# Kernel optimization log

Measured on AMD Instinct MI355X. Metric: run time of the kernel, lower is better.

The kernel has to match this reference:

```python
import jax, jax.numpy as jnp
import numpy as np

B, N, D, H = 2, 2048, 1024, 16
DH = D // H
SCALE = 1.0 / np.sqrt(DH).astype(np.float32)


def setup_inputs() -> dict:
    key = jax.random.key(0)
    k1, k2, k3, k4, k5 = jax.random.split(key, 5)
    x = jax.random.normal(k1, (B, N, D), dtype=jnp.float32)
    attn_bias = jax.random.normal(k2, (B, N, N), dtype=jnp.float32)
    # valid lengths in [N//2, N]; True = keep
    lengths = jax.random.randint(k3, (B,), N // 2, N + 1)
    key_padding_mask = jnp.arange(N)[None, :] < lengths[:, None]
    Wqkv = jax.random.normal(k4, (3 * D, D), dtype=jnp.float32) / np.sqrt(D)
    Wproj = jax.random.normal(k5, (D, D), dtype=jnp.float32) / np.sqrt(D)
    bproj = jnp.zeros((D,), dtype=jnp.float32)
    return {"x": x, "attn_bias": attn_bias, "key_padding_mask": key_padding_mask,
            "Wqkv": Wqkv, "Wproj": Wproj, "bproj": bproj}


def reference(x, attn_bias, key_padding_mask, Wqkv, Wproj, bproj):
    b, n, d = x.shape
    qkv = x @ Wqkv.T                                   # [B,N,3D]
    qkv = qkv.reshape(b, n, 3, H, DH)
    q = jnp.transpose(qkv[:, :, 0], (0, 2, 1, 3))      # [B,H,N,DH]
    k = jnp.transpose(qkv[:, :, 1], (0, 2, 1, 3))
    v = jnp.transpose(qkv[:, :, 2], (0, 2, 1, 3))
    attn = jnp.einsum('bhnd,bhmd->bhnm', q, k) * SCALE  # [B,H,N,N]
    attn = attn + attn_bias[:, None, :, :]
    attn = jnp.where(key_padding_mask[:, None, None, :], attn, -jnp.inf)
    attn = jax.nn.softmax(attn, axis=-1)
    y = jnp.einsum('bhnm,bhmd->bhnd', attn, v)          # [B,H,N,DH]
    y = jnp.transpose(y, (0, 2, 1, 3)).reshape(b, n, d)
    return y @ Wproj.T + bproj
```

## Files before the change

kernel.cpp:

```cpp
#include <hip/hip_runtime.h>
#include <hip/hip_bf16.h>

namespace {

typedef short short8 __attribute__((ext_vector_type(8)));
typedef float f32x4 __attribute__((ext_vector_type(4)));

__device__ __forceinline__ unsigned short f2bf(float f) {
  union { __hip_bfloat16 h; unsigned short u; } cv;
  cv.h = __float2bfloat16(f);
  return cv.u;
}

__device__ __forceinline__ unsigned cvt_pk_bf16(float lo, float hi) {
  unsigned r;
  asm("v_cvt_pk_bf16_f32 %0, %1, %2" : "=v"(r) : "v"(lo), "v"(hi));
  return r;
}

__device__ __forceinline__ void load_lds16(const void* g, void* l) {
  __builtin_amdgcn_global_load_lds((__attribute__((address_space(1))) void*)g,
                                   (__attribute__((address_space(3))) void*)l,
                                   16, 0, 0);
}

__device__ __forceinline__ int pi64(int rho) {
  const int c32 = rho & 32;
  const int o = (rho >> 4) & 1;
  const int g = (rho >> 2) & 3;
  const int s = rho & 3;
  return c32 + (o ? (((g ^ 2) << 3) + 4 + s) : ((g << 3) + s));
}

__global__ __launch_bounds__(256) void cvt_all(const float4* __restrict__ x,
                                               const float4* __restrict__ wqkv,
                                               const float4* __restrict__ wproj,
                                               ushort4* __restrict__ xb,
                                               ushort4* __restrict__ wqkvb,
                                               ushort4* __restrict__ wprojb) {
  int i = blockIdx.x * 256 + threadIdx.x;
  const float4* src;
  ushort4* dst;
  int off;
  if (i < 1048576) { src = x; dst = xb; off = i; }
  else if (i < 1048576 + 786432) { src = wqkv; dst = wqkvb; off = i - 1048576; }
  else { src = wproj; dst = wprojb; off = i - (1048576 + 786432); }
  float4 f = src[off];
  ushort4 u;
  u.x = f2bf(f.x); u.y = f2bf(f.y); u.z = f2bf(f.z); u.w = f2bf(f.w);
  dst[off] = u;
}

__global__ __launch_bounds__(256) void gemm_qkv(const unsigned short* __restrict__ Xb,
                                                const unsigned short* __restrict__ Wb,
                                                unsigned short* __restrict__ qws,
                                                unsigned short* __restrict__ kws,
                                                unsigned short* __restrict__ vTws) {
  __shared__ unsigned short lA[128 * 32];
  __shared__ unsigned short lB[128 * 32];
  const int t = threadIdx.x;
  const int w = t >> 6, l = t & 63;
  const int wm = w >> 1, wn = w & 1;
  const int lr = l & 15, lg = l >> 4;
  const int row0 = blockIdx.x * 128, col0 = blockIdx.y * 128;
  const int srow = t >> 2;
  const int schunk = (t & 3) ^ (srow & 3);
  f32x4 acc[4][4] = {};
  for (int k0 = 0; k0 < 1024; k0 += 32) {
    __syncthreads();
    load_lds16(Xb + (size_t)(row0 + srow) * 1024 + k0 + schunk * 8, &lA[w * 512]);
    load_lds16(Xb + (size_t)(row0 + 64 + srow) * 1024 + k0 + schunk * 8, &lA[2048 + w * 512]);
    load_lds16(Wb + (size_t)(col0 + srow) * 1024 + k0 + schunk * 8, &lB[w * 512]);
    load_lds16(Wb + (size_t)(col0 + 64 + srow) * 1024 + k0 + schunk * 8, &lB[2048 + w * 512]);
    __syncthreads();
    short8 af[4], bf[4];
    const int rslot = (lg ^ (l & 3)) * 8;
#pragma unroll
    for (int mi = 0; mi < 4; ++mi)
      af[mi] = *(const short8*)&lA[(wm * 64 + mi * 16 + lr) * 32 + rslot];
#pragma unroll
    for (int ni = 0; ni < 4; ++ni)
      bf[ni] = *(const short8*)&lB[(wn * 64 + ni * 16 + lr) * 32 + rslot];
#pragma unroll
    for (int mi = 0; mi < 4; ++mi)
#pragma unroll
      for (int ni = 0; ni < 4; ++ni)
        acc[mi][ni] = __builtin_amdgcn_mfma_f32_16x16x32_bf16(af[mi], bf[ni], acc[mi][ni], 0, 0, 0);
  }
#pragma unroll
  for (int mi = 0; mi < 4; ++mi)
#pragma unroll
    for (int ni = 0; ni < 4; ++ni) {
      const int col = col0 + wn * 64 + ni * 16 + lr;
      const int s = col >> 10, rem = col & 1023;
      const int hh = rem >> 6, dh = rem & 63;
      const int row = row0 + wm * 64 + mi * 16 + lg * 4;
      const int bb = row >> 11, n = row & 2047;
      const size_t bh = (size_t)(bb * 16 + hh);
      if (s == 2) {
        ushort4 u4;
        u4.x = f2bf(acc[mi][ni][0]); u4.y = f2bf(acc[mi][ni][1]);
        u4.z = f2bf(acc[mi][ni][2]); u4.w = f2bf(acc[mi][ni][3]);
        *(ushort4*)&vTws[(bh * 64 + dh) * 2048 + n] = u4;
      } else if (s == 0) {
#pragma unroll
        for (int r = 0; r < 4; ++r)
          qws[(bh * 2048 + n + r) * 64 + dh] = f2bf(acc[mi][ni][r] * 0.125f);
      } else {
#pragma unroll
        for (int r = 0; r < 4; ++r)
          kws[(bh * 2048 + n + r) * 64 + dh] = f2bf(acc[mi][ni][r]);
      }
    }
}

__global__ __launch_bounds__(256, 4) void attn_fwd(const unsigned short* __restrict__ qws,
                                                   const unsigned short* __restrict__ kws,
                                                   const unsigned short* __restrict__ vTws,
                                                   const float* __restrict__ bias,
                                                   const int* __restrict__ mask,
                                                   unsigned short* __restrict__ ctx) {
  __shared__ unsigned short lK[2][64 * 64];
  __shared__ unsigned short lVT[2][64 * 64];
  __shared__ int lred[4];
  const int t = threadIdx.x, w = t >> 6, l = t & 63;
  const int lr = l & 15, lg = l >> 4;
  const int xr7 = lr & 7;

  const int lin = blockIdx.x;
  const int g8 = lin & 7;
  const int k7 = lin >> 3;
  const int h = k7 & 15;
  const int gg = g8 + (k7 >> 4) * 8;
  const int qt = gg >> 1;
  const int b = gg & 1;

  const size_t bh = (size_t)(b * 16 + h);
  const unsigned short* Q = qws + bh * (2048 * 64);
  const unsigned short* K = kws + bh * (2048 * 64);
  const unsigned short* VT = vTws + bh * (64 * 2048);
  const float* brow = bias + (size_t)b * (2048 * 2048);

  const int* mrow = mask + b * 2048;
  int scnt = 0;
  for (int i = t; i < 2048; i += 256) scnt += (mrow[i] != 0);
#pragma unroll
  for (int d = 1; d < 64; d <<= 1) scnt += __shfl_xor(scnt, d, 64);
  if (l == 0) lred[w] = scnt;
  __syncthreads();
  const int len = lred[0] + lred[1] + lred[2] + lred[3];
  const int nt = (len + 63) >> 6;

  const int qv = qt * 64 + w * 16 + lr;
  short8 qf[2];
  qf[0] = *(const short8*)&Q[(size_t)qv * 64 + lg * 8];
  qf[1] = *(const short8*)&Q[(size_t)qv * 64 + 32 + lg * 8];
  const float* bq = brow + (size_t)qv * 2048;

  const int be = lg * 8, bo = ((lg ^ 2) * 8) + 4;
  const int boffs[4] = {be, bo, 32 + be, 32 + bo};

  float m = -INFINITY, lsum = 0.f;
  f32x4 o[4] = {};

  const int sr = l >> 3;
  const int sc7 = l & 7;

  float4 b4[4];
#pragma unroll
  for (int u = 0; u < 2; ++u) {
    const int row = w * 16 + u * 8 + sr;
    const int srcc = (sc7 ^ sr) * 8;
    load_lds16(K + (size_t)pi64(row) * 64 + srcc, &lK[0][(w * 16 + u * 8) * 64]);
    load_lds16(VT + (size_t)row * 2048 + srcc, &lVT[0][(w * 16 + u * 8) * 64]);
  }
#pragma unroll
  for (int j = 0; j < 4; ++j) b4[j] = *(const float4*)&bq[boffs[j]];
  __syncthreads();

  for (int ti = 0;;) {
    const int cur = ti & 1;
    const int kt = ti << 6;
    const bool notlast = (ti + 1 < nt);
    float4 b4n[4];
    if (notlast) {
      const int ktn = kt + 64;
#pragma unroll
      for (int u = 0; u < 2; ++u) {
        const int row = w * 16 + u * 8 + sr;
        const int srcc = (sc7 ^ sr) * 8;
        load_lds16(K + (size_t)(ktn + pi64(row)) * 64 + srcc, &lK[cur ^ 1][(w * 16 + u * 8) * 64]);
        load_lds16(VT + (size_t)row * 2048 + ktn + srcc, &lVT[cur ^ 1][(w * 16 + u * 8) * 64]);
      }
#pragma unroll
      for (int j = 0; j < 4; ++j) b4n[j] = *(const float4*)&bq[ktn + boffs[j]];
    }

    f32x4 s4[4];
#pragma unroll
    for (int j = 0; j < 4; ++j) {
      f32x4 sj = {0.f, 0.f, 0.f, 0.f};
      const int krow = (j * 16 + lr) * 64;
      short8 kf0 = *(const short8*)&lK[cur][krow + (lg ^ xr7) * 8];
      short8 kf1 = *(const short8*)&lK[cur][krow + ((lg + 4) ^ xr7) * 8];
      sj = __builtin_amdgcn_mfma_f32_16x16x32_bf16(kf0, qf[0], sj, 0, 0, 0);
      sj = __builtin_amdgcn_mfma_f32_16x16x32_bf16(kf1, qf[1], sj, 0, 0, 0);
      s4[j] = sj;
    }
    if (kt + 64 <= len) {
#pragma unroll
      for (int j = 0; j < 4; ++j) {
        s4[j][0] += b4[j].x; s4[j][1] += b4[j].y;
        s4[j][2] += b4[j].z; s4[j][3] += b4[j].w;
      }
    } else {
#pragma unroll
      for (int j = 0; j < 4; ++j) {
        const int kb = kt + boffs[j];
        const float* bp = &b4[j].x;
#pragma unroll
        for (int r = 0; r < 4; ++r)
          s4[j][r] = (kb + r < len) ? (s4[j][r] + bp[r]) : -1e30f;
      }
    }
    float rl = -1e30f;
#pragma unroll
    for (int j = 0; j < 4; ++j)
#pragma unroll
      for (int r = 0; r < 4; ++r) rl = fmaxf(rl, s4[j][r]);
    rl = fmaxf(rl, __shfl_xor(rl, 16, 64));
    rl = fmaxf(rl, __shfl_xor(rl, 32, 64));
    const float mn = fmaxf(m, rl);
    const float alpha = __expf(m - mn);
    m = mn;
    float rs = 0.f;
#pragma unroll
    for (int j = 0; j < 4; ++j)
#pragma unroll
      for (int r = 0; r < 4; ++r) {
        float p = __expf(s4[j][r] - m);
        s4[j][r] = p;
        rs += p;
      }
    rs += __shfl_xor(rs, 16, 64);
    rs += __shfl_xor(rs, 32, 64);
    lsum = lsum * alpha + rs;
    float ash[4];
#pragma unroll
    for (int r = 0; r < 4; ++r) ash[r] = __shfl(alpha, lg * 4 + r, 16);
#pragma unroll
    for (int ni = 0; ni < 4; ++ni)
#pragma unroll
      for (int r = 0; r < 4; ++r) o[ni][r] *= ash[r];

    unsigned wj0[4], wj1[4];
#pragma unroll
    for (int j = 0; j < 4; ++j) {
      wj0[j] = cvt_pk_bf16(s4[j][0], s4[j][1]);
      wj1[j] = cvt_pk_bf16(s4[j][2], s4[j][3]);
    }
#pragma unroll
    for (int c = 0; c < 2; ++c) {
      union { unsigned u[4]; short8 s8; } pu;
      pu.u[0] = wj0[2 * c];
      pu.u[1] = wj1[2 * c];
      pu.u[2] = (unsigned)__shfl_xor((int)wj0[2 * c + 1], 32, 64);
      pu.u[3] = (unsigned)__shfl_xor((int)wj1[2 * c + 1], 32, 64);
#pragma unroll
      for (int ni = 0; ni < 4; ++ni) {
        short8 vf = *(const short8*)&lVT[cur][(ni * 16 + lr) * 64 + ((c * 4 + lg) ^ xr7) * 8];
        o[ni] = __builtin_amdgcn_mfma_f32_16x16x32_bf16(pu.s8, vf, o[ni], 0, 0, 0);
      }
    }
    if (!notlast) break;
#pragma unroll
    for (int j = 0; j < 4; ++j) b4[j] = b4n[j];
    __syncthreads();
    ++ti;
  }
  float linv[4];
#pragma unroll
  for (int r = 0; r < 4; ++r) linv[r] = 1.0f / __shfl(lsum, lg * 4 + r, 16);
#pragma unroll
  for (int r = 0; r < 4; ++r) {
    const size_t orow = (size_t)b * 2048 + qt * 64 + w * 16 + lg * 4 + r;
#pragma unroll
    for (int ni = 0; ni < 4; ++ni)
      ctx[orow * 1024 + h * 64 + ni * 16 + lr] = f2bf(o[ni][r] * linv[r]);
  }
}

__global__ __launch_bounds__(256) void gemm_proj(const unsigned short* __restrict__ Cb,
                                                 const unsigned short* __restrict__ Wb,
                                                 const float* __restrict__ bproj,
                                                 float* __restrict__ out) {
  __shared__ unsigned short lA[128 * 32];
  __shared__ unsigned short lB[128 * 32];
  const int t = threadIdx.x;
  const int w = t >> 6, l = t & 63;
  const int wm = w >> 1, wn = w & 1;
  const int lr = l & 15, lg = l >> 4;
  const int row0 = blockIdx.x * 128, col0 = blockIdx.y * 128;
  const int srow = t >> 2;
  const int schunk = (t & 3) ^ (srow & 3);
  f32x4 acc[4][4] = {};
  for (int k0 = 0; k0 < 1024; k0 += 32) {
    __syncthreads();
    load_lds16(Cb + (size_t)(row0 + srow) * 1024 + k0 + schunk * 8, &lA[w * 512]);
    load_lds16(Cb + (size_t)(row0 + 64 + srow) * 1024 + k0 + schunk * 8, &lA[2048 + w * 512]);
    load_lds16(Wb + (size_t)(col0 + srow) * 1024 + k0 + schunk * 8, &lB[w * 512]);
    load_lds16(Wb + (size_t)(col0 + 64 + srow) * 1024 + k0 + schunk * 8, &lB[2048 + w * 512]);
    __syncthreads();
    short8 af[4], bf[4];
    const int rslot = (lg ^ (l & 3)) * 8;
#pragma unroll
    for (int mi = 0; mi < 4; ++mi)
      af[mi] = *(const short8*)&lA[(wm * 64 + mi * 16 + lr) * 32 + rslot];
#pragma unroll
    for (int ni = 0; ni < 4; ++ni)
      bf[ni] = *(const short8*)&lB[(wn * 64 + ni * 16 + lr) * 32 + rslot];
#pragma unroll
    for (int mi = 0; mi < 4; ++mi)
#pragma unroll
      for (int ni = 0; ni < 4; ++ni)
        acc[mi][ni] = __builtin_amdgcn_mfma_f32_16x16x32_bf16(af[mi], bf[ni], acc[mi][ni], 0, 0, 0);
  }
#pragma unroll
  for (int mi = 0; mi < 4; ++mi)
#pragma unroll
    for (int ni = 0; ni < 4; ++ni) {
      const int col = col0 + wn * 64 + ni * 16 + lr;
      const float bp = bproj[col];
#pragma unroll
      for (int r = 0; r < 4; ++r) {
        const int row = row0 + wm * 64 + mi * 16 + lg * 4 + r;
        out[(size_t)row * 1024 + col] = acc[mi][ni][r] + bp;
      }
    }
}

}

extern "C" void kernel_launch(void* const* d_in, const int* in_sizes, int n_in,
                              void* d_out, int out_size, void* d_ws, size_t ws_size,
                              hipStream_t stream) {
  (void)in_sizes; (void)n_in; (void)out_size; (void)ws_size;
  const float* x        = (const float*)d_in[0];
  const float* attnbias = (const float*)d_in[1];
  const int*   mask     = (const int*)d_in[2];
  const float* Wqkv     = (const float*)d_in[3];
  const float* Wproj    = (const float*)d_in[4];
  const float* bproj    = (const float*)d_in[5];
  float* out = (float*)d_out;

  unsigned short* ws     = (unsigned short*)d_ws;
  unsigned short* xb     = ws;
  unsigned short* wqkvb  = xb + 4194304;
  unsigned short* wprojb = wqkvb + 3145728;
  unsigned short* qws    = wprojb + 1048576;
  unsigned short* kws    = qws + 4194304;
  unsigned short* vTws   = kws + 4194304;
  unsigned short* ctxb   = vTws + 4194304;

  cvt_all<<<8192, 256, 0, stream>>>((const float4*)x, (const float4*)Wqkv,
                                    (const float4*)Wproj, (ushort4*)xb,
                                    (ushort4*)wqkvb, (ushort4*)wprojb);
  gemm_qkv<<<dim3(32, 24), 256, 0, stream>>>(xb, wqkvb, qws, kws, vTws);
  attn_fwd<<<1024, 256, 0, stream>>>(qws, kws, vTws, attnbias, mask, ctxb);
  gemm_proj<<<dim3(32, 8), 256, 0, stream>>>(ctxb, wprojb, bproj, out);
}
```

Measured before the change: 156.1 us.

## Restructure attention kernel: 512-thread blocks, 4-slot K/V pipeline, lazy rescale, exp2

Each attention block now covers 128 query rows with 8 waves and 512 threads. K/V tiles go through a 4-slot LDS ring that stages two tiles at once, with one barrier per pair of tiles. The log2(e) factor is folded into the Q scale and the bias FMA so exp2 can replace exp. The running max is rescaled only when it grows by more than a threshold, and the row sum comes from an extra MFMA against a ones vector instead of shuffle reductions. The tile count is rounded up to an even number, so one extra fully masked tile may be computed, and the manual vmcnt waits depend on the exact instruction counts.

```diff
diff --git a/kernel.cpp b/kernel.cpp
--- a/kernel.cpp
+++ b/kernel.cpp
@@ -5,6 +5,9 @@
 
 typedef short short8 __attribute__((ext_vector_type(8)));
 typedef float f32x4 __attribute__((ext_vector_type(4)));
+
+#define L2E 1.4426950408889634f
+#define SB() __builtin_amdgcn_sched_barrier(0)
 
 __device__ __forceinline__ unsigned short f2bf(float f) {
   union { __hip_bfloat16 h; unsigned short u; } cv;
@@ -105,7 +108,7 @@
       } else if (s == 0) {
 #pragma unroll
         for (int r = 0; r < 4; ++r)
-          qws[(bh * 2048 + n + r) * 64 + dh] = f2bf(acc[mi][ni][r] * 0.125f);
+          qws[(bh * 2048 + n + r) * 64 + dh] = f2bf(acc[mi][ni][r] * 0.18033688011112042f);
       } else {
 #pragma unroll
         for (int r = 0; r < 4; ++r)
@@ -114,26 +117,26 @@
     }
 }
 
-__global__ __launch_bounds__(256, 4) void attn_fwd(const unsigned short* __restrict__ qws,
+__global__ __launch_bounds__(512, 4) void attn_fwd(const unsigned short* __restrict__ qws,
                                                    const unsigned short* __restrict__ kws,
                                                    const unsigned short* __restrict__ vTws,
                                                    const float* __restrict__ bias,
                                                    const int* __restrict__ mask,
                                                    unsigned short* __restrict__ ctx) {
-  __shared__ unsigned short lK[2][64 * 64];
-  __shared__ unsigned short lVT[2][64 * 64];
-  __shared__ int lred[4];
+  __shared__ unsigned short lK[4][64 * 64];
+  __shared__ unsigned short lVT[4][64 * 64];
+  __shared__ int lred[8];
   const int t = threadIdx.x, w = t >> 6, l = t & 63;
   const int lr = l & 15, lg = l >> 4;
   const int xr7 = lr & 7;
 
   const int lin = blockIdx.x;
-  const int g8 = lin & 7;
-  const int k7 = lin >> 3;
-  const int h = k7 & 15;
-  const int gg = g8 + (k7 >> 4) * 8;
-  const int qt = gg >> 1;
-  const int b = gg & 1;
+  const int xcd = lin & 7;
+  const int idx = lin >> 3;
+  const int h = idx & 15;
+  const int q5 = idx >> 4;
+  const int b = q5 >> 1;
+  const int qt = xcd + 8 * (q5 & 1);
 
   const size_t bh = (size_t)(b * 16 + h);
   const unsigned short* Q = qws + bh * (2048 * 64);
@@ -143,75 +146,70 @@
 
   const int* mrow = mask + b * 2048;
   int scnt = 0;
-  for (int i = t; i < 2048; i += 256) scnt += (mrow[i] != 0);
+#pragma unroll
+  for (int i = 0; i < 4; ++i) scnt += (mrow[t + i * 512] != 0);
 #pragma unroll
   for (int d = 1; d < 64; d <<= 1) scnt += __shfl_xor(scnt, d, 64);
   if (l == 0) lred[w] = scnt;
   __syncthreads();
-  const int len = lred[0] + lred[1] + lred[2] + lred[3];
-  const int nt = (len + 63) >> 6;
-
-  const int qv = qt * 64 + w * 16 + lr;
-  short8 qf[2];
-  qf[0] = *(const short8*)&Q[(size_t)qv * 64 + lg * 8];
-  qf[1] = *(const short8*)&Q[(size_t)qv * 64 + 32 + lg * 8];
+  int len = 0;
+#pragma unroll
+  for (int i = 0; i < 8; ++i) len += lred[i];
+  const int nt = ((((len + 63) >> 6) + 1) & ~1);
+
+  const int qv = qt * 128 + w * 16 + lr;
+  const short8 qf0 = *(const short8*)&Q[(size_t)qv * 64 + lg * 8];
+  const short8 qf1 = *(const short8*)&Q[(size_t)qv * 64 + 32 + lg * 8];
   const float* bq = brow + (size_t)qv * 2048;
 
   const int be = lg * 8, bo = ((lg ^ 2) * 8) + 4;
   const int boffs[4] = {be, bo, 32 + be, 32 + bo};
 
-  float m = -INFINITY, lsum = 0.f;
-  f32x4 o[4] = {};
+  short8 vones;
+#pragma unroll
+  for (int i = 0; i < 8; ++i) vones[i] = (short)0x3F80;
+
+  float m = -INFINITY;
+  f32x4 o[5] = {};
 
   const int sr = l >> 3;
-  const int sc7 = l & 7;
-
-  float4 b4[4];
-#pragma unroll
-  for (int u = 0; u < 2; ++u) {
-    const int row = w * 16 + u * 8 + sr;
-    const int srcc = (sc7 ^ sr) * 8;
-    load_lds16(K + (size_t)pi64(row) * 64 + srcc, &lK[0][(w * 16 + u * 8) * 64]);
-    load_lds16(VT + (size_t)row * 2048 + srcc, &lVT[0][(w * 16 + u * 8) * 64]);
-  }
-#pragma unroll
-  for (int j = 0; j < 4; ++j) b4[j] = *(const float4*)&bq[boffs[j]];
-  __syncthreads();
-
-  for (int ti = 0;;) {
-    const int cur = ti & 1;
+  const int sc = ((l & 7) ^ sr) * 8;
+  const int krow8 = w * 8 + sr;
+
+  auto STAGE = [&](int ti2) {
+    const int slot = ti2 & 3;
+    const int kt2 = ti2 << 6;
+    load_lds16(K + (size_t)(kt2 + pi64(krow8)) * 64 + sc, &lK[slot][w * 512]);
+    load_lds16(VT + (size_t)krow8 * 2048 + kt2 + sc, &lVT[slot][w * 512]);
+  };
+  auto LOADB = [&](float4 (&d)[4], int ti2) {
+    const int kt2 = ti2 << 6;
+#pragma unroll
+    for (int j = 0; j < 4; ++j) d[j] = *(const float4*)&bq[kt2 + boffs[j]];
+  };
+  auto COMPUTE = [&](int ti, float4 (&b4)[4]) {
+    const int slot = ti & 3;
     const int kt = ti << 6;
-    const bool notlast = (ti + 1 < nt);
-    float4 b4n[4];
-    if (notlast) {
-      const int ktn = kt + 64;
-#pragma unroll
-      for (int u = 0; u < 2; ++u) {
-        const int row = w * 16 + u * 8 + sr;
-        const int srcc = (sc7 ^ sr) * 8;
-        load_lds16(K + (size_t)(ktn + pi64(row)) * 64 + srcc, &lK[cur ^ 1][(w * 16 + u * 8) * 64]);
-        load_lds16(VT + (size_t)row * 2048 + ktn + srcc, &lVT[cur ^ 1][(w * 16 + u * 8) * 64]);
-      }
-#pragma unroll
-      for (int j = 0; j < 4; ++j) b4n[j] = *(const float4*)&bq[ktn + boffs[j]];
-    }
-
+    const unsigned short* lKs = lK[slot];
+    const unsigned short* lVs = lVT[slot];
     f32x4 s4[4];
 #pragma unroll
     for (int j = 0; j < 4; ++j) {
       f32x4 sj = {0.f, 0.f, 0.f, 0.f};
       const int krow = (j * 16 + lr) * 64;
-      short8 kf0 = *(const short8*)&lK[cur][krow + (lg ^ xr7) * 8];
-      short8 kf1 = *(const short8*)&lK[cur][krow + ((lg + 4) ^ xr7) * 8];
-      sj = __builtin_amdgcn_mfma_f32_16x16x32_bf16(kf0, qf[0], sj, 0, 0, 0);
-      sj = __builtin_amdgcn_mfma_f32_16x16x32_bf16(kf1, qf[1], sj, 0, 0, 0);
+      short8 kf0 = *(const short8*)&lKs[krow + (lg ^ xr7) * 8];
+      short8 kf1 = *(const short8*)&lKs[krow + ((lg + 4) ^ xr7) * 8];
+      sj = __builtin_amdgcn_mfma_f32_16x16x32_bf16(kf0, qf0, sj, 0, 0, 0);
+      sj = __builtin_amdgcn_mfma_f32_16x16x32_bf16(kf1, qf1, sj, 0, 0, 0);
       s4[j] = sj;
     }
     if (kt + 64 <= len) {
 #pragma unroll
       for (int j = 0; j < 4; ++j) {
-        s4[j][0] += b4[j].x; s4[j][1] += b4[j].y;
-        s4[j][2] += b4[j].z; s4[j][3] += b4[j].w;
+        s4[j][0] = fmaf(b4[j].x, L2E, s4[j][0]);
+        s4[j][1] = fmaf(b4[j].y, L2E, s4[j][1]);
+        s4[j][2] = fmaf(b4[j].z, L2E, s4[j][2]);
+        s4[j][3] = fmaf(b4[j].w, L2E, s4[j][3]);
       }
     } else {
 #pragma unroll
@@ -220,39 +218,35 @@
         const float* bp = &b4[j].x;
 #pragma unroll
         for (int r = 0; r < 4; ++r)
-          s4[j][r] = (kb + r < len) ? (s4[j][r] + bp[r]) : -1e30f;
-      }
-    }
-    float rl = -1e30f;
+          s4[j][r] = (kb + r < len) ? fmaf(bp[r], L2E, s4[j][r]) : -1e30f;
+      }
+    }
+    f32x4 m01, m23;
+#pragma unroll
+    for (int r = 0; r < 4; ++r) {
+      m01[r] = fmaxf(s4[0][r], s4[1][r]);
+      m23[r] = fmaxf(s4[2][r], s4[3][r]);
+      m01[r] = fmaxf(m01[r], m23[r]);
+    }
+    float rl = fmaxf(fmaxf(m01[0], m01[1]), fmaxf(m01[2], m01[3]));
+    if (!__all(rl - m <= 12.0f)) {
+      rl = fmaxf(rl, __shfl_xor(rl, 16, 64));
+      rl = fmaxf(rl, __shfl_xor(rl, 32, 64));
+      const float mn = fmaxf(m, rl);
+      const float al = exp2f(m - mn);
+      m = mn;
+      float ash[4];
+#pragma unroll
+      for (int r = 0; r < 4; ++r) ash[r] = __shfl(al, lg * 4 + r, 16);
+#pragma unroll
+      for (int ni = 0; ni < 5; ++ni)
+#pragma unroll
+        for (int r = 0; r < 4; ++r) o[ni][r] *= ash[r];
+    }
 #pragma unroll
     for (int j = 0; j < 4; ++j)
 #pragma unroll
-      for (int r = 0; r < 4; ++r) rl = fmaxf(rl, s4[j][r]);
-    rl = fmaxf(rl, __shfl_xor(rl, 16, 64));
-    rl = fmaxf(rl, __shfl_xor(rl, 32, 64));
-    const float mn = fmaxf(m, rl);
-    const float alpha = __expf(m - mn);
-    m = mn;
-    float rs = 0.f;
-#pragma unroll
-    for (int j = 0; j < 4; ++j)
-#pragma unroll
-      for (int r = 0; r < 4; ++r) {
-        float p = __expf(s4[j][r] - m);
-        s4[j][r] = p;
-        rs += p;
-      }
-    rs += __shfl_xor(rs, 16, 64);
-    rs += __shfl_xor(rs, 32, 64);
-    lsum = lsum * alpha + rs;
-    float ash[4];
-#pragma unroll
-    for (int r = 0; r < 4; ++r) ash[r] = __shfl(alpha, lg * 4 + r, 16);
-#pragma unroll
-    for (int ni = 0; ni < 4; ++ni)
-#pragma unroll
-      for (int r = 0; r < 4; ++r) o[ni][r] *= ash[r];
-
+      for (int r = 0; r < 4; ++r) s4[j][r] = exp2f(s4[j][r] - m);
     unsigned wj0[4], wj1[4];
 #pragma unroll
     for (int j = 0; j < 4; ++j) {
@@ -268,22 +262,50 @@
       pu.u[3] = (unsigned)__shfl_xor((int)wj1[2 * c + 1], 32, 64);
 #pragma unroll
       for (int ni = 0; ni < 4; ++ni) {
-        short8 vf = *(const short8*)&lVT[cur][(ni * 16 + lr) * 64 + ((c * 4 + lg) ^ xr7) * 8];
+        short8 vf = *(const short8*)&lVs[(ni * 16 + lr) * 64 + ((c * 4 + lg) ^ xr7) * 8];
         o[ni] = __builtin_amdgcn_mfma_f32_16x16x32_bf16(pu.s8, vf, o[ni], 0, 0, 0);
       }
-    }
-    if (!notlast) break;
-#pragma unroll
-    for (int j = 0; j < 4; ++j) b4[j] = b4n[j];
-    __syncthreads();
-    ++ti;
+      o[4] = __builtin_amdgcn_mfma_f32_16x16x32_bf16(pu.s8, vones, o[4], 0, 0, 0);
+    }
+  };
+
+  float4 bA[4], bB[4], bAn[4], bBn[4];
+  SB();
+  STAGE(0); STAGE(1);
+  SB();
+  LOADB(bA, 0); LOADB(bB, 1);
+  SB();
+  asm volatile("s_waitcnt vmcnt(8)" ::: "memory");
+  __builtin_amdgcn_s_barrier();
+  SB();
+
+  for (int ti = 0; ti < nt; ti += 2) {
+    const bool hn = (ti + 2 < nt);
+    if (hn) {
+      SB();
+      STAGE(ti + 2); STAGE(ti + 3);
+      SB();
+      LOADB(bAn, ti + 2); LOADB(bBn, ti + 3);
+      SB();
+    }
+    COMPUTE(ti, bA);
+    COMPUTE(ti + 1, bB);
+    if (hn) {
+#pragma unroll
+      for (int j = 0; j < 4; ++j) { bA[j] = bAn[j]; bB[j] = bBn[j]; }
+      SB();
+      asm volatile("s_waitcnt vmcnt(8) lgkmcnt(0)" ::: "memory");
+      __builtin_amdgcn_s_barrier();
+      SB();
+    }
   }
+
   float linv[4];
 #pragma unroll
-  for (int r = 0; r < 4; ++r) linv[r] = 1.0f / __shfl(lsum, lg * 4 + r, 16);
+  for (int r = 0; r < 4; ++r) linv[r] = 1.0f / o[4][r];
 #pragma unroll
   for (int r = 0; r < 4; ++r) {
-    const size_t orow = (size_t)b * 2048 + qt * 64 + w * 16 + lg * 4 + r;
+    const size_t orow = (size_t)b * 2048 + qt * 128 + w * 16 + lg * 4 + r;
 #pragma unroll
     for (int ni = 0; ni < 4; ++ni)
       ctx[orow * 1024 + h * 64 + ni * 16 + lr] = f2bf(o[ni][r] * linv[r]);
@@ -366,6 +388,6 @@
                                     (const float4*)Wproj, (ushort4*)xb,
                                     (ushort4*)wqkvb, (ushort4*)wprojb);
   gemm_qkv<<<dim3(32, 24), 256, 0, stream>>>(xb, wqkvb, qws, kws, vTws);
-  attn_fwd<<<1024, 256, 0, stream>>>(qws, kws, vTws, attnbias, mask, ctxb);
+  attn_fwd<<<512, 512, 0, stream>>>(qws, kws, vTws, attnbias, mask, ctxb);
   gemm_proj<<<dim3(32, 8), 256, 0, stream>>>(ctxb, wprojb, bproj, out);
 }
```

Result: slower. 204.9 us (+31.2%).
